# Performance work log

Measured on AMD Instinct MI355X. Metric: run time of the kernel, lower is better.

The kernel has to match this reference:

```python
import jax, jax.numpy as jnp
import numpy as np

WIN = 9  # window_size (isotropic, module default)
EPS = 1e-5


def _box_sum3d(x, win):
    """Sum over a win^3 box, same-size output ('same' padding). x: [B,1,D,H,W].
    The ones kernel is separable, so apply three 1D convolutions."""
    pad = win // 2
    for ax in range(3):  # spatial axes D,H,W
        kshape = [1, 1, 1, 1, 1]
        kshape[2 + ax] = win
        k = jnp.ones(kshape, x.dtype)
        padding = [(0, 0)] * 3
        padding[ax] = (pad, pad)
        x = jax.lax.conv_general_dilated(x, k, window_strides=(1, 1, 1), padding=padding)
    return x


def setup_inputs() -> dict:
    key = jax.random.key(0)
    k1, k2 = jax.random.split(key)
    shape = (2, 1, 160, 192, 160)
    y_pred = jax.random.normal(k1, shape, dtype=jnp.float32)
    y_true = jax.random.normal(k2, shape, dtype=jnp.float32)
    return {"y_pred": y_pred, "y_true": y_true}


def reference(y_pred, y_true):
    I, J = y_true, y_pred
    win_size = jnp.asarray(WIN ** 3, I.dtype)  # 729

    I_sum = _box_sum3d(I, WIN)
    J_sum = _box_sum3d(J, WIN)
    I2_sum = _box_sum3d(I * I, WIN)
    J2_sum = _box_sum3d(J * J, WIN)
    IJ_sum = _box_sum3d(I * J, WIN)

    I_mean = I_sum / win_size
    J_mean = J_sum / win_size

    cross = IJ_sum - J_mean * I_sum - I_mean * J_sum + I_mean * J_mean * win_size
    I_var = I2_sum - 2 * I_mean * I_sum + I_mean * I_mean * win_size
    J_var = J2_sum - 2 * J_mean * J_sum + J_mean * J_mean * win_size

    cc = cross * cross / (I_var * J_var + EPS)
    return -jnp.mean(cc)
```

## Files before the change

### kernel.cpp

```cpp
#include <hip/hip_runtime.h>
#include <hip/hip_fp16.h>


#define B_    2
#define D_    160
#define H_    192
#define W_    160
#define HW_   (H_*W_)

#define RS    12
#define SLS   (24*RS)
#define FS    (2*SLS)
#define ZROW  (5*FS)
#define TMP0  (ZROW + 16)
#define TS    18
#define HSUM0 (TMP0 + 4*16*TS)
#define HCS   160
#define HRS   10
#define REDU  (HSUM0 + 10*HCS)
#define SMEM  (REDU + 8)
#define DC    20
#define ZCH   (D_/DC)
#define NMAC  ((DC+8)/2)
#define W3I   (1.0f/729.0f)
#define NTOT  9830400.0f

#if __has_builtin(__builtin_amdgcn_rcpf)
#define RCP(x) __builtin_amdgcn_rcpf(x)
#else
#define RCP(x) (1.0f/(x))
#endif
#define LGKM0() asm volatile("s_waitcnt lgkmcnt(0)" ::: "memory")

typedef _Float16 half8 __attribute__((ext_vector_type(8)));
typedef float    f32x4 __attribute__((ext_vector_type(4)));
#define MFMA16(a,b,c) __builtin_amdgcn_mfma_f32_16x16x32_f16((a),(b),(c),0,0,0)

struct __align__(8) HP { __half2 a, b; };

__global__ __launch_bounds__(256, 4) void ncc_fused(const float* __restrict__ gI,
                                                    const float* __restrict__ gJ,
                                                    float* __restrict__ out)
{
  __shared__ __align__(16) float sm[SMEM];
  const int tid  = threadIdx.x;
  const int lane = tid & 63;
  const int Q    = tid >> 6;
  const int n15  = lane & 15;
  const int q4   = lane >> 4;
  const int w0   = blockIdx.x * 16;
  const int h0   = blockIdx.y * 16;
  const int bz   = blockIdx.z;
  const int bb   = bz / ZCH;
  const int d_lo = (bz % ZCH) * DC;

  for (int i = tid; i < TMP0; i += 256) sm[i] = 0.f;

  half8 SEL;
  #pragma unroll
  for (int j = 0; j < 8; ++j) {
    const int k = 8*q4 + j;
    SEL[j] = (k >= n15 && k <= n15 + 8) ? (_Float16)1 : (_Float16)0;
  }

  bool val0 = false, val1 = false;
  int  lo0 = 0, lo1 = 0, sc0 = 0, sc1 = 0;
  const float *pi0 = gI, *pj0 = gJ, *pi1 = gI, *pj1 = gJ;
  {
    auto prep = [&](int t, bool& val, int& lo, int& sc,
                    const float*& pi, const float*& pj) {
      if (t >= 288) { val = false; return; }
      sc = t / 144;
      const int u = t - sc*144;
      const int r = u / 6, c = u - r*6;
      const int gh = h0 - 4 + r, gw = w0 - 4 + 4*c;
      val = ((unsigned)gh < (unsigned)H_) && (gw >= 0) && (gw + 3 < W_);
      lo  = sc*SLS + r*RS + 2*c;
      const long off = ((long)(bb*D_ + (d_lo - 4 + sc))*H_ + gh)*(long)W_ + gw;
      pi = gI + off; pj = gJ + off;
    };
    prep(tid, val0, lo0, sc0, pi0, pj0);
    prep((tid >= 224) ? tid + 32 : 512, val1, lo1, sc1, pi1, pj1);
  }

  int rb_[3], hb_[3];
  #pragma unroll
  for (int i = 0; i < 3; ++i) {
    int c = Q + 4*i; if (c > 9) c = 9;
    rb_[i] = (c % 5)*FS + (c / 5)*SLS;
    hb_[i] = HSUM0 + c*HCS;
  }
  const int tb  = TMP0 + Q*(16*TS) + n15*TS;
  const int a1r = n15*RS + 4*q4;
  const int a2r = (n15 < 8) ? ((16 + n15)*RS + 4*q4) : -1;
  const int zr  = ZROW + 4*q4;

  const int rh = tid >> 4, rw = tid & 15;
  const int rbase = HSUM0 + rw*HRS + (rh >> 1);
  const int rsh   = (rh & 1) * 16;

  float ring[5][9], S[5];
  #pragma unroll
  for (int f = 0; f < 5; ++f) {
    S[f] = 0.f;
    #pragma unroll
    for (int k = 0; k < 9; ++k) ring[f][k] = 0.f;
  }
  float acc = 0.f;

  float4 f0i = {0,0,0,0}, f0j = {0,0,0,0}, f1i = {0,0,0,0}, f1j = {0,0,0,0};
  auto fetch = [&](int sbase) {
    if (val0 && (unsigned)(sbase + sc0) < (unsigned)D_) {
      f0i = *(const float4*)pi0; f0j = *(const float4*)pj0;
    } else { f0i = make_float4(0,0,0,0); f0j = make_float4(0,0,0,0); }
    pi0 += 2*HW_; pj0 += 2*HW_;
    if (val1 && (unsigned)(sbase + sc1) < (unsigned)D_) {
      f1i = *(const float4*)pi1; f1j = *(const float4*)pj1;
    } else { f1i = make_float4(0,0,0,0); f1j = make_float4(0,0,0,0); }
    pi1 += 2*HW_; pj1 += 2*HW_;
  };

  auto stage_one = [&](int lo, float4 fi, float4 fj) {
    const __half2 i01 = __floats2half2_rn(fi.x, fi.y);
    const __half2 i23 = __floats2half2_rn(fi.z, fi.w);
    const __half2 j01 = __floats2half2_rn(fj.x, fj.y);
    const __half2 j23 = __floats2half2_rn(fj.z, fj.w);
    HP hI; hI.a = i01; hI.b = i23;
    HP hJ; hJ.a = j01; hJ.b = j23;
    HP h2; h2.a = __hmul2(i01, i01); h2.b = __hmul2(i23, i23);
    HP h3; h3.a = __hmul2(j01, j01); h3.b = __hmul2(j23, j23);
    HP h4; h4.a = __hmul2(i01, j01); h4.b = __hmul2(i23, j23);
    *(HP*)&sm[lo]        = hI;
    *(HP*)&sm[lo +   FS] = hJ;
    *(HP*)&sm[lo + 2*FS] = h2;
    *(HP*)&sm[lo + 3*FS] = h3;
    *(HP*)&sm[lo + 4*FS] = h4;
  };
  auto stage_write = [&]() {
    if (val0) stage_one(lo0, f0i, f0j);
    if (val1) stage_one(lo1, f1i, f1j);
  };

  auto chain = [&](int rb, int hb) {
    const half8 A1 = *(const half8*)&sm[rb + a1r];
    const half8 A2 = (a2r >= 0) ? *(const half8*)&sm[rb + a2r]
                                : *(const half8*)&sm[zr];
    const f32x4 z = {0.f, 0.f, 0.f, 0.f};
    const f32x4 d1 = MFMA16(A1, SEL, z);
    const f32x4 d2 = MFMA16(A2, SEL, z);
    HP p1; p1.a = __floats2half2_rn(d1[0], d1[1]); p1.b = __floats2half2_rn(d1[2], d1[3]);
    HP p2; p2.a = __floats2half2_rn(d2[0], d2[1]); p2.b = __floats2half2_rn(d2[2], d2[3]);
    *(HP*)&sm[tb + 2*q4]     = p1;
    *(HP*)&sm[tb + 8 + 2*q4] = p2;
    LGKM0();
    const half8 Bh = *(const half8*)&sm[tb + 4*q4];
    const f32x4 dh = MFMA16(SEL, Bh, z);
    HP ph; ph.a = __floats2half2_rn(dh[0], dh[1]); ph.b = __floats2half2_rn(dh[2], dh[3]);
    *(HP*)&sm[hb + n15*HRS + 2*q4] = ph;
  };

  auto h2ext = [&](int addr) -> float {
    const unsigned u = *(const unsigned*)&sm[addr];
    return __half2float(__ushort_as_half((unsigned short)(u >> rsh)));
  };
  auto ring_cc = [&](int m) {
    float nA[5], nB[5];
    #pragma unroll
    for (int f = 0; f < 5; ++f) {
      nA[f] = h2ext(rbase + f*HCS);
      nB[f] = h2ext(rbase + (5 + f)*HCS);
    }
    float SA[5], SB[5];
    #pragma unroll
    for (int f = 0; f < 5; ++f) {
      SA[f] = S[f]  + nA[f] - ring[f][8];
      SB[f] = SA[f] + nB[f] - ring[f][7];
      S[f]  = SB[f];
      #pragma unroll
      for (int k = 8; k >= 2; --k) ring[f][k] = ring[f][k-2];
      ring[f][1] = nA[f]; ring[f][0] = nB[f];
    }
    if (m >= 4) {
      {
        const float cr = SA[4] - SA[0]*SA[1]*W3I;
        const float vi = SA[2] - SA[0]*SA[0]*W3I;
        const float vj = SA[3] - SA[1]*SA[1]*W3I;
        acc += cr*cr * RCP(vi*vj + 1e-5f);
      }
      {
        const float cr = SB[4] - SB[0]*SB[1]*W3I;
        const float vi = SB[2] - SB[0]*SB[0]*W3I;
        const float vj = SB[3] - SB[1]*SB[1]*W3I;
        acc += cr*cr * RCP(vi*vj + 1e-5f);
      }
    }
  };

  fetch(d_lo - 4);
  __syncthreads();
  stage_write();
  fetch(d_lo - 2);
  __syncthreads();

  for (int m = 0; m < NMAC; ++m) {
    chain(rb_[0], hb_[0]);
    chain(rb_[1], hb_[1]);
    if (Q < 2) chain(rb_[2], hb_[2]);
    __syncthreads();
    if (m + 1 < NMAC) { stage_write(); fetch(d_lo + 2*m); }
    ring_cc(m);
    __syncthreads();
  }

  float v = acc;
  #pragma unroll
  for (int off = 32; off > 0; off >>= 1)
    v += __shfl_down(v, off, 64);
  if (lane == 0) sm[REDU + Q] = v;
  __syncthreads();
  if (tid == 0) {
    const float t = sm[REDU] + sm[REDU+1] + sm[REDU+2] + sm[REDU+3];
    atomicAdd(out, -t / NTOT);
  }
}

extern "C" void kernel_launch(void* const* d_in, const int* in_sizes, int n_in,
                              void* d_out, int out_size, void* d_ws, size_t ws_size,
                              hipStream_t stream) {
  const float* J = (const float*)d_in[0];
  const float* I = (const float*)d_in[1];
  float* outp = (float*)d_out;
  hipMemsetAsync(d_out, 0, sizeof(float), stream);
  dim3 grid(W_/16, H_/16, B_*ZCH);
  ncc_fused<<<grid, dim3(256), 0, stream>>>(I, J, outp);
}
```

Before: 164.6 us.

## Replace LDS transpose with permlane swaps and double depth chunk size

The intermediate MFMA result is no longer written to a shared-memory scratch tile and read back transposed. Instead it is rearranged across lanes with permlane32/permlane16 swap instructions, which removes the LDS round trip and its wait, and shrinks the shared-memory footprint. The depth chunk per block also doubles from 20 to 40. That halves the grid and cuts the redundant 8-slice halo loads per chunk, at the cost of fewer blocks to fill the GPU. The lane permutation must reproduce the old transpose layout exactly for the result to stay correct.

```diff
diff --git a/kernel.cpp b/kernel.cpp
--- a/kernel.cpp
+++ b/kernel.cpp
@@ -12,14 +12,13 @@
 #define SLS   (24*RS)
 #define FS    (2*SLS)
 #define ZROW  (5*FS)
-#define TMP0  (ZROW + 16)
-#define TS    18
-#define HSUM0 (TMP0 + 4*16*TS)
+#define ZEND  (ZROW + 16)
+#define HSUM0 ZEND
 #define HCS   160
 #define HRS   10
 #define REDU  (HSUM0 + 10*HCS)
 #define SMEM  (REDU + 8)
-#define DC    20
+#define DC    40
 #define ZCH   (D_/DC)
 #define NMAC  ((DC+8)/2)
 #define W3I   (1.0f/729.0f)
@@ -30,11 +29,24 @@
 #else
 #define RCP(x) (1.0f/(x))
 #endif
-#define LGKM0() asm volatile("s_waitcnt lgkmcnt(0)" ::: "memory")
 
 typedef _Float16 half8 __attribute__((ext_vector_type(8)));
 typedef float    f32x4 __attribute__((ext_vector_type(4)));
+typedef unsigned u32x2 __attribute__((ext_vector_type(2)));
 #define MFMA16(a,b,c) __builtin_amdgcn_mfma_f32_16x16x32_f16((a),(b),(c),0,0,0)
+
+#if __has_builtin(__builtin_amdgcn_permlane32_swap)
+#define PL32(a,b) do { u32x2 _s = __builtin_amdgcn_permlane32_swap((a),(b),false,false); \
+                       (a)=_s[0]; (b)=_s[1]; } while(0)
+#else
+#define PL32(a,b) asm volatile("s_nop 1\nv_permlane32_swap_b32 %0, %1" : "+v"(a), "+v"(b))
+#endif
+#if __has_builtin(__builtin_amdgcn_permlane16_swap)
+#define PL16(a,b) do { u32x2 _s = __builtin_amdgcn_permlane16_swap((a),(b),false,false); \
+                       (a)=_s[0]; (b)=_s[1]; } while(0)
+#else
+#define PL16(a,b) asm volatile("s_nop 1\nv_permlane16_swap_b32 %0, %1" : "+v"(a), "+v"(b))
+#endif
 
 struct __align__(8) HP { __half2 a, b; };
 
@@ -54,7 +66,7 @@
   const int bb   = bz / ZCH;
   const int d_lo = (bz % ZCH) * DC;
 
-  for (int i = tid; i < TMP0; i += 256) sm[i] = 0.f;
+  for (int i = tid; i < ZEND; i += 256) sm[i] = 0.f;
 
   half8 SEL;
   #pragma unroll
@@ -90,7 +102,6 @@
     rb_[i] = (c % 5)*FS + (c / 5)*SLS;
     hb_[i] = HSUM0 + c*HCS;
   }
-  const int tb  = TMP0 + Q*(16*TS) + n15*TS;
   const int a1r = n15*RS + 4*q4;
   const int a2r = (n15 < 8) ? ((16 + n15)*RS + 4*q4) : -1;
   const int zr  = ZROW + 4*q4;
@@ -148,13 +159,17 @@
     const f32x4 z = {0.f, 0.f, 0.f, 0.f};
     const f32x4 d1 = MFMA16(A1, SEL, z);
     const f32x4 d2 = MFMA16(A2, SEL, z);
-    HP p1; p1.a = __floats2half2_rn(d1[0], d1[1]); p1.b = __floats2half2_rn(d1[2], d1[3]);
-    HP p2; p2.a = __floats2half2_rn(d2[0], d2[1]); p2.b = __floats2half2_rn(d2[2], d2[3]);
-    *(HP*)&sm[tb + 2*q4]     = p1;
-    *(HP*)&sm[tb + 8 + 2*q4] = p2;
-    LGKM0();
-    const half8 Bh = *(const half8*)&sm[tb + 4*q4];
-    const f32x4 dh = MFMA16(SEL, Bh, z);
+    unsigned t0 = __builtin_bit_cast(unsigned, __floats2half2_rn(d1[0], d1[1]));
+    unsigned t1 = __builtin_bit_cast(unsigned, __floats2half2_rn(d1[2], d1[3]));
+    unsigned u0 = __builtin_bit_cast(unsigned, __floats2half2_rn(d2[0], d2[1]));
+    unsigned u1 = __builtin_bit_cast(unsigned, __floats2half2_rn(d2[2], d2[3]));
+    PL32(t0, u0);
+    PL32(t1, u1);
+    PL16(t0, u0);
+    PL16(t1, u1);
+    union { unsigned u[4]; half8 h; } Bv;
+    Bv.u[0] = t0; Bv.u[1] = t1; Bv.u[2] = u0; Bv.u[3] = u1;
+    const f32x4 dh = MFMA16(SEL, Bv.h, z);
     HP ph; ph.a = __floats2half2_rn(dh[0], dh[1]); ph.b = __floats2half2_rn(dh[2], dh[3]);
     *(HP*)&sm[hb + n15*HRS + 2*q4] = ph;
   };
```

After: 147.4 us. -10.4%, faster.
